# Performance work log

Hardware: AMD Instinct MI355X
Metric: run time of the kernel (lower is better)

## Reference

```python
import jax, jax.numpy as jnp
import numpy as np

NUM_EXPERTS = 8
HIDDEN = 2048
INTER = 1408
TOKENS = 2048
TOP_K = 2


def setup_inputs() -> dict:
    key = jax.random.key(0)
    ks = jax.random.split(key, 6)
    s_h = 1.0 / np.sqrt(HIDDEN)
    s_i = 1.0 / np.sqrt(INTER)
    hidden_states = jax.random.normal(ks[0], (TOKENS, HIDDEN), dtype=jnp.float32)
    top_k_index = jax.random.randint(ks[1], (TOKENS, TOP_K), 0, NUM_EXPERTS)
    w = jax.random.uniform(ks[2], (TOKENS, TOP_K), dtype=jnp.float32)
    top_k_weights = w / jnp.sum(w, axis=-1, keepdims=True)
    # weights stored as [E, in, out] for einsum (torch Linear is [out, in])
    gate_w = jax.random.uniform(ks[3], (NUM_EXPERTS, HIDDEN, INTER), jnp.float32, -s_h, s_h)
    up_w = jax.random.uniform(ks[4], (NUM_EXPERTS, HIDDEN, INTER), jnp.float32, -s_h, s_h)
    down_w = jax.random.uniform(ks[5], (NUM_EXPERTS, INTER, HIDDEN), jnp.float32, -s_i, s_i)
    return {
        "hidden_states": hidden_states,
        "top_k_index": top_k_index,
        "top_k_weights": top_k_weights,
        "gate_w": gate_w,
        "up_w": up_w,
        "down_w": down_w,
    }


def reference(hidden_states, top_k_index, top_k_weights, gate_w, up_w, down_w):
    # combine weight per (expert, token): w_et = sum_k topk_w[t,k] * [idx[t,k]==e]
    one_hot = jax.nn.one_hot(top_k_index, NUM_EXPERTS, dtype=hidden_states.dtype)  # [T,K,E]
    combine = jnp.einsum("tk,tke->et", top_k_weights, one_hot)  # [E,T]
    # dense per-expert SwiGLU MLP over all tokens (mask-combine form of the
    # gather/scatter loop; identical math since combine weight is 0 for
    # non-routed (expert, token) pairs)
    g = jnp.einsum("th,ehi->eti", hidden_states, gate_w)  # [E,T,I]
    u = jnp.einsum("th,ehi->eti", hidden_states, up_w)
    y = jnp.einsum("eti,eih->eth", jax.nn.silu(g) * u, down_w)  # [E,T,H]
    out = jnp.einsum("et,eth->th", combine, y)  # [T,H]
    return out
```

## Files before the change

### kernel.cpp

```cpp
#include <hip/hip_runtime.h>
#include <cstdint>
#include <cstddef>

#define NE 8
#define HD 2048
#define IN 1408
#define NT 2048
#define NP (NT*2)
#define MAXMT 40

typedef __bf16 bf16;
typedef __bf16 bf16x8 __attribute__((ext_vector_type(8)));
typedef __bf16 bf16x4 __attribute__((ext_vector_type(4)));
typedef float f32x4 __attribute__((ext_vector_type(4)));

__device__ __forceinline__ void load_lds16(const void* g, void* l) {
  __builtin_amdgcn_global_load_lds((const __attribute__((address_space(1))) uint32_t*)g,
                                   (__attribute__((address_space(3))) uint32_t*)l, 16, 0, 0);
}

#define PIPE_BAR() do { \
    asm volatile("s_waitcnt vmcnt(0) lgkmcnt(0)" ::: "memory"); \
    __builtin_amdgcn_s_barrier(); \
    __builtin_amdgcn_sched_barrier(0); \
  } while (0)

__global__ void k_cvt(const float* __restrict__ x, bf16* __restrict__ y) {
  int i = blockIdx.x * 256 + threadIdx.x;
  f32x4 v = ((const f32x4*)x)[i];
  bf16x4 o;
  o[0] = (bf16)v[0]; o[1] = (bf16)v[1]; o[2] = (bf16)v[2]; o[3] = (bf16)v[3];
  ((bf16x4*)y)[i] = o;
}

__global__ void k_route(const int* __restrict__ idx, const float* __restrict__ w,
                        int* __restrict__ perm_tok, float* __restrict__ perm_w,
                        int* __restrict__ slot_of, int* __restrict__ tiles) {
  __shared__ int cnt[NE], off[NE + 1], rk[NE];
  int tid = threadIdx.x;
  if (tid < NE) { cnt[tid] = 0; rk[tid] = 0; }
  __syncthreads();
  for (int a = tid; a < NP; a += 256) atomicAdd(&cnt[idx[a]], 1);
  __syncthreads();
  if (tid == 0) { off[0] = 0; for (int e = 0; e < NE; e++) off[e + 1] = off[e] + cnt[e]; }
  __syncthreads();
  for (int a = tid; a < NP; a += 256) {
    int e = idx[a];
    int p = off[e] + atomicAdd(&rk[e], 1);
    perm_tok[p] = a >> 1;
    perm_w[p] = w[a];
    slot_of[a] = p;
  }
  __syncthreads();
  if (tid == 0) {
    int n = 0;
    for (int e = 0; e < NE; e++)
      for (int r = off[e]; r < off[e + 1]; r += 128) {
        tiles[n] = e; tiles[MAXMT + n] = r; tiles[2 * MAXMT + n] = off[e + 1];
        n++;
      }
    for (int s = n; s < MAXMT; s++) tiles[s] = -1;
  }
}

template<int KTOT, int NTOT, bool GATHER>
__device__ __forceinline__ void mm_pipe(const bf16* __restrict__ A,
                                        const float* __restrict__ Bsrc,
                                        const int* __restrict__ perm_tok,
                                        int row0, int rowend, int nb,
                                        float* __restrict__ C) {
  __shared__ __align__(16) bf16 As[2][128 * 64];
  __shared__ __align__(16) bf16 Bs[2][128 * 64];

  int tid = threadIdx.x;
  int lane = tid & 63, wave = tid >> 6;
  int wm = (wave >> 1) * 64, wn = (wave & 1) * 64;

  const bf16* aG[4]; int aOff[4];
#pragma unroll
  for (int i2 = 0; i2 < 4; i2++) {
    int s = i2 * 256 + tid;
    int r = s >> 3, c = (s & 7) ^ (r & 7);
    int tr = row0 + r; if (tr > NP - 1) tr = NP - 1;
    int arow = GATHER ? perm_tok[tr] : tr;
    aG[i2] = A + (size_t)arow * KTOT + c * 8;
    aOff[i2] = s * 8;
  }
  int kk = (tid & 7) * 8, nn = (tid >> 3) * 4;
  const float* gB = Bsrc + (size_t)kk * NTOT + (nb + nn);
  int bslot[4];
#pragma unroll
  for (int i2 = 0; i2 < 4; i2++) { int n = nn + i2; bslot[i2] = (n * 8 + ((tid & 7) ^ (n & 7))) * 8; }

  f32x4 acc[4][4] = {};
  f32x4 v[8];

#pragma unroll
  for (int i2 = 0; i2 < 4; i2++) load_lds16(aG[i2], &As[0][aOff[i2]]);
#pragma unroll
  for (int j = 0; j < 8; j++) v[j] = *(const f32x4*)(gB + (size_t)j * NTOT);
#pragma unroll
  for (int i2 = 0; i2 < 4; i2++) {
    bf16x8 o;
#pragma unroll
    for (int j = 0; j < 8; j++) o[j] = (bf16)v[j][i2];
    *(bf16x8*)(&Bs[0][bslot[i2]]) = o;
  }
  PIPE_BAR();

  const int NK = KTOT / 64;
  int cur = 0;
#pragma unroll 2
  for (int k = 0; k < NK; k++) {
    if (k + 1 < NK) {
      int k0n = (k + 1) * 64;
#pragma unroll
      for (int j = 0; j < 8; j++) v[j] = *(const f32x4*)(gB + (size_t)(k0n + j) * NTOT);
#pragma unroll
      for (int i2 = 0; i2 < 4; i2++) load_lds16(aG[i2] + k0n, &As[cur ^ 1][aOff[i2]]);
    }
#pragma unroll
    for (int ks = 0; ks < 2; ks++) {
      int ckf = ks * 4 + (lane >> 4);
      bf16x8 af[4], bfr[4];
#pragma unroll
      for (int fm = 0; fm < 4; fm++) {
        int m = wm + fm * 16 + (lane & 15);
        af[fm] = *(const bf16x8*)(&As[cur][(m * 8 + (ckf ^ (m & 7))) * 8]);
      }
#pragma unroll
      for (int fn = 0; fn < 4; fn++) {
        int n = wn + fn * 16 + (lane & 15);
        bfr[fn] = *(const bf16x8*)(&Bs[cur][(n * 8 + (ckf ^ (n & 7))) * 8]);
      }
      __builtin_amdgcn_s_setprio(1);
#pragma unroll
      for (int fm = 0; fm < 4; fm++)
#pragma unroll
        for (int fn = 0; fn < 4; fn++)
          acc[fm][fn] = __builtin_amdgcn_mfma_f32_16x16x32_bf16(af[fm], bfr[fn], acc[fm][fn], 0, 0, 0);
      __builtin_amdgcn_s_setprio(0);
    }
    if (k + 1 < NK) {
#pragma unroll
      for (int i2 = 0; i2 < 4; i2++) {
        bf16x8 o;
#pragma unroll
        for (int j = 0; j < 8; j++) o[j] = (bf16)v[j][i2];
        *(bf16x8*)(&Bs[cur ^ 1][bslot[i2]]) = o;
      }
    }
    PIPE_BAR();
    cur ^= 1;
  }

#pragma unroll
  for (int fm = 0; fm < 4; fm++) {
#pragma unroll
    for (int rr = 0; rr < 4; rr++) {
      int m = wm + fm * 16 + ((lane >> 4) << 2) + rr;
      int row = row0 + m;
      if (row < rowend) {
#pragma unroll
        for (int fn = 0; fn < 4; fn++) {
          int n = nb + wn + fn * 16 + (lane & 15);
          C[(size_t)row * NTOT + n] = acc[fm][fn][rr];
        }
      }
    }
  }
}

__launch_bounds__(256, 2)
__global__ void k_mm1(const bf16* __restrict__ hid, const float* __restrict__ gw,
                      const float* __restrict__ uw, const int* __restrict__ perm_tok,
                      const int* __restrict__ tiles,
                      float* __restrict__ g, float* __restrict__ u) {
  int b = blockIdx.x;
  int half = b >= 440 ? 1 : 0;
  int b2 = b - half * 440;
  int slot = b2 / 11, nt = b2 % 11;
  int e = tiles[slot];
  if (e < 0) return;
  int row0 = tiles[MAXMT + slot], rowend = tiles[2 * MAXMT + slot];
  const float* B = (half ? uw : gw) + (size_t)e * HD * IN;
  float* C = half ? u : g;
  mm_pipe<HD, IN, true>(hid, B, perm_tok, row0, rowend, nt * 128, C);
}

__global__ void k_act(const float* __restrict__ g, const float* __restrict__ u,
                      const float* __restrict__ pw, bf16* __restrict__ act) {
  int i = blockIdx.x * 256 + threadIdx.x;
  int row = i / (IN / 8);
  float w = pw[row];
  f32x4 g0 = ((const f32x4*)g)[2 * i], g1 = ((const f32x4*)g)[2 * i + 1];
  f32x4 u0 = ((const f32x4*)u)[2 * i], u1 = ((const f32x4*)u)[2 * i + 1];
  bf16x8 o;
#pragma unroll
  for (int j = 0; j < 4; j++) {
    float s = g0[j] / (1.0f + __expf(-g0[j]));
    o[j] = (bf16)(s * u0[j] * w);
  }
#pragma unroll
  for (int j = 0; j < 4; j++) {
    float s = g1[j] / (1.0f + __expf(-g1[j]));
    o[4 + j] = (bf16)(s * u1[j] * w);
  }
  ((bf16x8*)act)[i] = o;
}

__launch_bounds__(256, 2)
__global__ void k_mm2(const bf16* __restrict__ act, const float* __restrict__ dw,
                      const int* __restrict__ tiles, float* __restrict__ pout) {
  int b = blockIdx.x;
  int slot = b >> 4, nt = b & 15;
  int e = tiles[slot];
  if (e < 0) return;
  int row0 = tiles[MAXMT + slot], rowend = tiles[2 * MAXMT + slot];
  mm_pipe<IN, HD, false>(act, dw + (size_t)e * IN * HD, nullptr, row0, rowend, nt * 128, pout);
}

__global__ void k_comb(const float* __restrict__ pout, const int* __restrict__ slot_of,
                       float* __restrict__ out) {
  int i = blockIdx.x * 256 + threadIdx.x;
  int t = i >> 9;
  int hc = i & 511;
  f32x4 a = ((const f32x4*)(pout + (size_t)slot_of[2 * t] * HD))[hc];
  f32x4 c = ((const f32x4*)(pout + (size_t)slot_of[2 * t + 1] * HD))[hc];
  ((f32x4*)(out + (size_t)t * HD))[hc] = a + c;
}

extern "C" void kernel_launch(void* const* d_in, const int* in_sizes, int n_in,
                              void* d_out, int out_size, void* d_ws, size_t ws_size,
                              hipStream_t stream) {
  const float* hidden  = (const float*)d_in[0];
  const int*   tk_idx  = (const int*)d_in[1];
  const float* tk_w    = (const float*)d_in[2];
  const float* gw      = (const float*)d_in[3];
  const float* uw      = (const float*)d_in[4];
  const float* dw      = (const float*)d_in[5];
  float* out = (float*)d_out;

  char* ws = (char*)d_ws;
  int*   perm_tok = (int*)ws;
  float* perm_w   = (float*)(ws + 16384);
  int*   slot_of  = (int*)(ws + 32768);
  int*   tiles    = (int*)(ws + 49152);
  bf16*  hid_bf   = (bf16*)(ws + 53248);
  bf16*  act      = (bf16*)(ws + 53248 + 8388608);
  char*  xbase    = ws + 53248 + 8388608 + 11534336;
  float* gbuf     = (float*)xbase;
  float* ubuf     = (float*)(xbase + 23068672);
  float* pout     = (float*)xbase;

  k_cvt  <<<4096, 256, 0, stream>>>(hidden, hid_bf);
  k_route<<<1,    256, 0, stream>>>(tk_idx, tk_w, perm_tok, perm_w, slot_of, tiles);
  k_mm1  <<<880,  256, 0, stream>>>(hid_bf, gw, uw, perm_tok, tiles, gbuf, ubuf);
  k_act  <<<2816, 256, 0, stream>>>(gbuf, ubuf, perm_w, act);
  k_mm2  <<<640,  256, 0, stream>>>(act, dw, tiles, pout);
  k_comb <<<4096, 256, 0, stream>>>(pout, slot_of, out);
}
```

Measured before the change: 496.8 us.

## Deepen GEMM B-prefetch pipeline and remap blocks for XCD-local expert reuse

Restructures the GEMM main loop to prefetch B (fp32 weights) two k-steps ahead using ping-pong register sets, with partial vmcnt waits instead of full drains each iteration. Adds a routing-built block map and an XCD-aware block index remap so that blocks sharing an expert's weight columns land on the same XCD and reuse its L2. Also compacts launches by skipping empty tile slots. This costs more registers and could lower occupancy.

```diff
diff --git a/kernel.cpp b/kernel.cpp
--- a/kernel.cpp
+++ b/kernel.cpp
@@ -19,12 +19,6 @@
                                    (__attribute__((address_space(3))) uint32_t*)l, 16, 0, 0);
 }
 
-#define PIPE_BAR() do { \
-    asm volatile("s_waitcnt vmcnt(0) lgkmcnt(0)" ::: "memory"); \
-    __builtin_amdgcn_s_barrier(); \
-    __builtin_amdgcn_sched_barrier(0); \
-  } while (0)
-
 __global__ void k_cvt(const float* __restrict__ x, bf16* __restrict__ y) {
   int i = blockIdx.x * 256 + threadIdx.x;
   f32x4 v = ((const f32x4*)x)[i];
@@ -35,8 +29,9 @@
 
 __global__ void k_route(const int* __restrict__ idx, const float* __restrict__ w,
                         int* __restrict__ perm_tok, float* __restrict__ perm_w,
-                        int* __restrict__ slot_of, int* __restrict__ tiles) {
-  __shared__ int cnt[NE], off[NE + 1], rk[NE];
+                        int* __restrict__ slot_of, int* __restrict__ tiles,
+                        int* __restrict__ bmap1, int* __restrict__ bmap2) {
+  __shared__ int cnt[NE], off[NE + 1], rk[NE], sb[NE + 1];
   int tid = threadIdx.x;
   if (tid < NE) { cnt[tid] = 0; rk[tid] = 0; }
   __syncthreads();
@@ -60,8 +55,68 @@
         n++;
       }
     for (int s = n; s < MAXMT; s++) tiles[s] = -1;
-  }
-}
+    tiles[3 * MAXMT] = n;
+    int a = 0;
+    for (int e = 0; e < NE; e++) { sb[e] = a; a += (cnt[e] + 127) >> 7; }
+    sb[NE] = a;
+  }
+  __syncthreads();
+  if (tid < NE) {
+    int e = tid, s0 = sb[e], s1 = sb[e + 1];
+    int j1 = s0 * 11, j2 = s0 * 16;
+    for (int nt = 0; nt < 11; nt++)
+      for (int s = s0; s < s1; s++) bmap1[j1++] = s | (nt << 16);
+    for (int nt = 0; nt < 16; nt++)
+      for (int s = s0; s < s1; s++) bmap2[j2++] = s | (nt << 16);
+  }
+}
+
+#define MM_COMPUTE(kk) do { \
+    const bf16* Ab_ = As + ((kk) & 1) * (128 * 64); \
+    const bf16* Bb_ = Bs + ((kk) & 1) * (128 * 64); \
+    _Pragma("unroll") \
+    for (int ks = 0; ks < 2; ks++) { \
+      int ckf = ks * 4 + (lane >> 4); \
+      bf16x8 af[4], bfr[4]; \
+      _Pragma("unroll") \
+      for (int fm = 0; fm < 4; fm++) { \
+        int m_ = wm + fm * 16 + (lane & 15); \
+        af[fm] = *(const bf16x8*)(Ab_ + (m_ * 8 + (ckf ^ (m_ & 7))) * 8); \
+      } \
+      _Pragma("unroll") \
+      for (int fn = 0; fn < 4; fn++) { \
+        int n_ = wn + fn * 16 + (lane & 15); \
+        bfr[fn] = *(const bf16x8*)(Bb_ + (n_ * 8 + (ckf ^ (n_ & 7))) * 8); \
+      } \
+      __builtin_amdgcn_s_setprio(1); \
+      _Pragma("unroll") \
+      for (int fm = 0; fm < 4; fm++) \
+        _Pragma("unroll") \
+        for (int fn = 0; fn < 4; fn++) \
+          acc[fm][fn] = __builtin_amdgcn_mfma_f32_16x16x32_bf16(af[fm], bfr[fn], acc[fm][fn], 0, 0, 0); \
+      __builtin_amdgcn_s_setprio(0); \
+    } \
+  } while (0)
+
+#define MM_BODY(kk, vCon, vLoad, WSTR) do { \
+    { int k0a = ((kk) + 1) * 64; \
+      bf16* dA_ = As + (((kk) + 1) & 1) * (128 * 64); \
+      _Pragma("unroll") \
+      for (int i2 = 0; i2 < 4; i2++) load_lds16(aG[i2] + k0a, dA_ + aOff[i2]); } \
+    __builtin_amdgcn_sched_barrier(0); \
+    if ((kk) + 2 < NK) { int k0b = ((kk) + 2) * 64; \
+      _Pragma("unroll") \
+      for (int j = 0; j < 8; j++) vLoad[j] = *(const f32x4*)(gB + (size_t)(k0b + j) * NTOT); } \
+    MM_COMPUTE(kk); \
+    { bf16* Bw_ = Bs + (((kk) + 1) & 1) * (128 * 64); \
+      _Pragma("unroll") \
+      for (int i2 = 0; i2 < 4; i2++) { bf16x8 o; \
+        _Pragma("unroll") for (int j = 0; j < 8; j++) o[j] = (bf16)vCon[j][i2]; \
+        *(bf16x8*)(Bw_ + bslot[i2]) = o; } } \
+    asm volatile("s_waitcnt " WSTR ::: "memory"); \
+    __builtin_amdgcn_s_barrier(); \
+    __builtin_amdgcn_sched_barrier(0); \
+  } while (0)
 
 template<int KTOT, int NTOT, bool GATHER>
 __device__ __forceinline__ void mm_pipe(const bf16* __restrict__ A,
@@ -69,8 +124,9 @@
                                         const int* __restrict__ perm_tok,
                                         int row0, int rowend, int nb,
                                         float* __restrict__ C) {
-  __shared__ __align__(16) bf16 As[2][128 * 64];
-  __shared__ __align__(16) bf16 Bs[2][128 * 64];
+  constexpr int NK = KTOT / 64;
+  __shared__ __align__(16) bf16 As[2 * 128 * 64];
+  __shared__ __align__(16) bf16 Bs[2 * 128 * 64];
 
   int tid = threadIdx.x;
   int lane = tid & 63, wave = tid >> 6;
@@ -86,73 +142,40 @@
     aG[i2] = A + (size_t)arow * KTOT + c * 8;
     aOff[i2] = s * 8;
   }
-  int kk = (tid & 7) * 8, nn = (tid >> 3) * 4;
-  const float* gB = Bsrc + (size_t)kk * NTOT + (nb + nn);
+  int kk0 = (tid & 7) * 8, nn = (tid >> 3) * 4;
+  const float* gB = Bsrc + (size_t)kk0 * NTOT + (nb + nn);
   int bslot[4];
 #pragma unroll
   for (int i2 = 0; i2 < 4; i2++) { int n = nn + i2; bslot[i2] = (n * 8 + ((tid & 7) ^ (n & 7))) * 8; }
 
   f32x4 acc[4][4] = {};
-  f32x4 v[8];
-
-#pragma unroll
-  for (int i2 = 0; i2 < 4; i2++) load_lds16(aG[i2], &As[0][aOff[i2]]);
-#pragma unroll
-  for (int j = 0; j < 8; j++) v[j] = *(const f32x4*)(gB + (size_t)j * NTOT);
+  f32x4 vA[8], vB[8];
+
+#pragma unroll
+  for (int i2 = 0; i2 < 4; i2++) load_lds16(aG[i2], As + aOff[i2]);
+  __builtin_amdgcn_sched_barrier(0);
+#pragma unroll
+  for (int j = 0; j < 8; j++) vA[j] = *(const f32x4*)(gB + (size_t)j * NTOT);
+#pragma unroll
+  for (int j = 0; j < 8; j++) vB[j] = *(const f32x4*)(gB + (size_t)(64 + j) * NTOT);
 #pragma unroll
   for (int i2 = 0; i2 < 4; i2++) {
     bf16x8 o;
 #pragma unroll
-    for (int j = 0; j < 8; j++) o[j] = (bf16)v[j][i2];
-    *(bf16x8*)(&Bs[0][bslot[i2]]) = o;
-  }
-  PIPE_BAR();
-
-  const int NK = KTOT / 64;
-  int cur = 0;
-#pragma unroll 2
-  for (int k = 0; k < NK; k++) {
-    if (k + 1 < NK) {
-      int k0n = (k + 1) * 64;
-#pragma unroll
-      for (int j = 0; j < 8; j++) v[j] = *(const f32x4*)(gB + (size_t)(k0n + j) * NTOT);
-#pragma unroll
-      for (int i2 = 0; i2 < 4; i2++) load_lds16(aG[i2] + k0n, &As[cur ^ 1][aOff[i2]]);
-    }
-#pragma unroll
-    for (int ks = 0; ks < 2; ks++) {
-      int ckf = ks * 4 + (lane >> 4);
-      bf16x8 af[4], bfr[4];
-#pragma unroll
-      for (int fm = 0; fm < 4; fm++) {
-        int m = wm + fm * 16 + (lane & 15);
-        af[fm] = *(const bf16x8*)(&As[cur][(m * 8 + (ckf ^ (m & 7))) * 8]);
-      }
-#pragma unroll
-      for (int fn = 0; fn < 4; fn++) {
-        int n = wn + fn * 16 + (lane & 15);
-        bfr[fn] = *(const bf16x8*)(&Bs[cur][(n * 8 + (ckf ^ (n & 7))) * 8]);
-      }
-      __builtin_amdgcn_s_setprio(1);
-#pragma unroll
-      for (int fm = 0; fm < 4; fm++)
-#pragma unroll
-        for (int fn = 0; fn < 4; fn++)
-          acc[fm][fn] = __builtin_amdgcn_mfma_f32_16x16x32_bf16(af[fm], bfr[fn], acc[fm][fn], 0, 0, 0);
-      __builtin_amdgcn_s_setprio(0);
-    }
-    if (k + 1 < NK) {
-#pragma unroll
-      for (int i2 = 0; i2 < 4; i2++) {
-        bf16x8 o;
-#pragma unroll
-        for (int j = 0; j < 8; j++) o[j] = (bf16)v[j][i2];
-        *(bf16x8*)(&Bs[cur ^ 1][bslot[i2]]) = o;
-      }
-    }
-    PIPE_BAR();
-    cur ^= 1;
-  }
+    for (int j = 0; j < 8; j++) o[j] = (bf16)vA[j][i2];
+    *(bf16x8*)(Bs + bslot[i2]) = o;
+  }
+  asm volatile("s_waitcnt vmcnt(8) lgkmcnt(0)" ::: "memory");
+  __builtin_amdgcn_s_barrier();
+  __builtin_amdgcn_sched_barrier(0);
+
+#pragma unroll 1
+  for (int k = 0; k + 2 < NK; k += 2) {
+    MM_BODY(k,     vB, vA, "vmcnt(8) lgkmcnt(0)");
+    MM_BODY(k + 1, vA, vB, "vmcnt(8) lgkmcnt(0)");
+  }
+  MM_BODY(NK - 2, vB, vA, "vmcnt(0) lgkmcnt(0)");
+  MM_COMPUTE(NK - 1);
 
 #pragma unroll
   for (int fm = 0; fm < 4; fm++) {
@@ -171,17 +194,27 @@
   }
 }
 
+__device__ __forceinline__ int xcd_logical(int b, int W) {
+  int xcd = b & 7, p = b >> 3;
+  int q = W >> 3, r = W & 7;
+  int cs = xcd < r ? q + 1 : q;
+  if (p >= cs) return -1;
+  return (xcd < r ? xcd * (q + 1) : r * (q + 1) + (xcd - r) * q) + p;
+}
+
 __launch_bounds__(256, 2)
 __global__ void k_mm1(const bf16* __restrict__ hid, const float* __restrict__ gw,
                       const float* __restrict__ uw, const int* __restrict__ perm_tok,
-                      const int* __restrict__ tiles,
+                      const int* __restrict__ tiles, const int* __restrict__ bmap1,
                       float* __restrict__ g, float* __restrict__ u) {
-  int b = blockIdx.x;
-  int half = b >= 440 ? 1 : 0;
-  int b2 = b - half * 440;
-  int slot = b2 / 11, nt = b2 % 11;
+  int nsl = tiles[3 * MAXMT];
+  int hn = 11 * nsl;
+  int l = xcd_logical(blockIdx.x, 2 * hn);
+  if (l < 0) return;
+  int half = l >= hn ? 1 : 0;
+  int m = bmap1[l - half * hn];
+  int slot = m & 0xffff, nt = m >> 16;
   int e = tiles[slot];
-  if (e < 0) return;
   int row0 = tiles[MAXMT + slot], rowend = tiles[2 * MAXMT + slot];
   const float* B = (half ? uw : gw) + (size_t)e * HD * IN;
   float* C = half ? u : g;
@@ -211,11 +244,14 @@
 
 __launch_bounds__(256, 2)
 __global__ void k_mm2(const bf16* __restrict__ act, const float* __restrict__ dw,
-                      const int* __restrict__ tiles, float* __restrict__ pout) {
-  int b = blockIdx.x;
-  int slot = b >> 4, nt = b & 15;
+                      const int* __restrict__ tiles, const int* __restrict__ bmap2,
+                      float* __restrict__ pout) {
+  int nsl = tiles[3 * MAXMT];
+  int l = xcd_logical(blockIdx.x, 16 * nsl);
+  if (l < 0) return;
+  int m = bmap2[l];
+  int slot = m & 0xffff, nt = m >> 16;
   int e = tiles[slot];
-  if (e < 0) return;
   int row0 = tiles[MAXMT + slot], rowend = tiles[2 * MAXMT + slot];
   mm_pipe<IN, HD, false>(act, dw + (size_t)e * IN * HD, nullptr, row0, rowend, nt * 128, pout);
 }
@@ -246,17 +282,19 @@
   float* perm_w   = (float*)(ws + 16384);
   int*   slot_of  = (int*)(ws + 32768);
   int*   tiles    = (int*)(ws + 49152);
-  bf16*  hid_bf   = (bf16*)(ws + 53248);
-  bf16*  act      = (bf16*)(ws + 53248 + 8388608);
-  char*  xbase    = ws + 53248 + 8388608 + 11534336;
+  int*   bmap1    = (int*)(ws + 50176);
+  int*   bmap2    = (int*)(ws + 52224);
+  bf16*  hid_bf   = (bf16*)(ws + 65536);
+  bf16*  act      = (bf16*)(ws + 65536 + 8388608);
+  char*  xbase    = ws + 65536 + 8388608 + 11534336;
   float* gbuf     = (float*)xbase;
   float* ubuf     = (float*)(xbase + 23068672);
   float* pout     = (float*)xbase;
 
   k_cvt  <<<4096, 256, 0, stream>>>(hidden, hid_bf);
-  k_route<<<1,    256, 0, stream>>>(tk_idx, tk_w, perm_tok, perm_w, slot_of, tiles);
-  k_mm1  <<<880,  256, 0, stream>>>(hid_bf, gw, uw, perm_tok, tiles, gbuf, ubuf);
+  k_route<<<1,    256, 0, stream>>>(tk_idx, tk_w, perm_tok, perm_w, slot_of, tiles, bmap1, bmap2);
+  k_mm1  <<<880,  256, 0, stream>>>(hid_bf, gw, uw, perm_tok, tiles, bmap1, gbuf, ubuf);
   k_act  <<<2816, 256, 0, stream>>>(gbuf, ubuf, perm_w, act);
-  k_mm2  <<<640,  256, 0, stream>>>(act, dw, tiles, pout);
+  k_mm2  <<<640,  256, 0, stream>>>(act, dw, tiles, bmap2, pout);
   k_comb <<<4096, 256, 0, stream>>>(pout, slot_of, out);
 }
```

Result: faster. 479.9 us (-3.4%).
